# Performance work log

Measured on AMD Instinct MI355X. Metric: run time of the kernel, lower is better.

The kernel has to match this reference:

```python
import jax, jax.numpy as jnp
import numpy as np

N = 50000
E = 800000
NODE_DIM = 128
EDGE_DIM = 64


def leaky_relu(x, slope=0.2):
    return jnp.where(x >= 0, x, slope * x)


def setup_inputs() -> dict:
    key = jax.random.key(0)
    ks = jax.random.split(key, 12)
    node_feats = jax.random.normal(ks[0], (N, NODE_DIM), dtype=jnp.float32)
    edge_index = jax.random.randint(ks[1], (2, E), 0, N, dtype=jnp.int64)
    edge_feats = jax.random.normal(ks[2], (E, EDGE_DIM), dtype=jnp.float32)
    # msg_mlp: Linear(node+edge -> node), LeakyReLU(0.2), Linear(node -> node)
    s1 = 1.0 / np.sqrt(NODE_DIM + EDGE_DIM)
    s2 = 1.0 / np.sqrt(NODE_DIM)
    s3 = 1.0 / np.sqrt(2 * NODE_DIM)
    msg_w1 = jax.random.uniform(ks[3], (NODE_DIM + EDGE_DIM, NODE_DIM), jnp.float32, -s1, s1)
    msg_b1 = jax.random.uniform(ks[4], (NODE_DIM,), jnp.float32, -s1, s1)
    msg_w2 = jax.random.uniform(ks[5], (NODE_DIM, NODE_DIM), jnp.float32, -s2, s2)
    msg_b2 = jax.random.uniform(ks[6], (NODE_DIM,), jnp.float32, -s2, s2)
    # update_mlp: Linear(2*node -> node), LeakyReLU(0.2), Linear(node -> node)
    upd_w1 = jax.random.uniform(ks[7], (2 * NODE_DIM, NODE_DIM), jnp.float32, -s3, s3)
    upd_b1 = jax.random.uniform(ks[8], (NODE_DIM,), jnp.float32, -s3, s3)
    upd_w2 = jax.random.uniform(ks[9], (NODE_DIM, NODE_DIM), jnp.float32, -s2, s2)
    upd_b2 = jax.random.uniform(ks[10], (NODE_DIM,), jnp.float32, -s2, s2)
    return {
        "node_feats": node_feats,
        "edge_feats": edge_feats,
        "msg_w1": msg_w1, "msg_b1": msg_b1, "msg_w2": msg_w2, "msg_b2": msg_b2,
        "upd_w1": upd_w1, "upd_b1": upd_b1, "upd_w2": upd_w2, "upd_b2": upd_b2,
        "edge_index": edge_index,
    }


def reference(node_feats, edge_feats, msg_w1, msg_b1, msg_w2, msg_b2,
              upd_w1, upd_b1, upd_w2, upd_b2, edge_index):
    src = edge_index[0]
    dst = edge_index[1]
    # gather neighbor features, concat with edge features: (E, node+edge)
    msg_input = jnp.concatenate([node_feats[dst], edge_feats], axis=1)
    h = leaky_relu(msg_input @ msg_w1 + msg_b1)
    messages = h @ msg_w2 + msg_b2                       # (E, node_dim)
    # scatter-add messages to source nodes
    aggregated = jax.ops.segment_sum(messages, src, num_segments=node_feats.shape[0])
    update_input = jnp.concatenate([node_feats, aggregated], axis=1)  # (N, 2*node_dim)
    h2 = leaky_relu(update_input @ upd_w1 + upd_b1)
    return h2 @ upd_w2 + upd_b2                          # (N, node_dim)
```

## Files before the change

### kernel.cpp

```cpp
#include <hip/hip_runtime.h>
#include <hip/hip_bf16.h>

#define NNODES 50000
#define NEDGES 800000
#define NDIM   128
#define EDIM   64
#define K1     192
#define K2     256
#define NB     196

#define KP1 200
#define KPA 136
#define KPU 264
#define MSTR 132

typedef __attribute__((ext_vector_type(8))) short bf16x8;
typedef __attribute__((ext_vector_type(4))) short bf16x4;
typedef __attribute__((ext_vector_type(4))) float f32x4;

__device__ inline short f2bf(float f) {
  union { float f; unsigned u; } v; v.f = f;
  unsigned r = v.u + 0x7FFFu + ((v.u >> 16) & 1u);
  return (short)(r >> 16);
}

__device__ inline bf16x4 pack4(float4 v) {
  bf16x4 p;
  p[0] = f2bf(v.x); p[1] = f2bf(v.y); p[2] = f2bf(v.z); p[3] = f2bf(v.w);
  return p;
}

__global__ __launch_bounds__(256) void cvt_kernel(const float* __restrict__ src,
                                                  short* __restrict__ dst, int n) {
  int i = (blockIdx.x * 256 + threadIdx.x) * 4;
  if (i < n) {
    float4 v = *(const float4*)(src + i);
    *(bf16x4*)(dst + i) = pack4(v);
  }
}

__global__ __launch_bounds__(256) void wt_all_kernel(const float* __restrict__ w1,
                                                     const float* __restrict__ w2,
                                                     const float* __restrict__ u1,
                                                     const float* __restrict__ u2,
                                                     short* __restrict__ w1t,
                                                     short* __restrict__ w2t,
                                                     short* __restrict__ u1t,
                                                     short* __restrict__ u2t) {
  int i = blockIdx.x * 256 + threadIdx.x;
  const int A0 = K1 * 128;
  const int A1 = A0 + 128 * 128;
  const int A2 = A1 + K2 * 128;
  const int A3 = A2 + 128 * 128;
  if (i < A0) {
    int j = i, k = j >> 7, n = j & 127;
    w1t[n * K1 + k] = f2bf(w1[j]);
  } else if (i < A1) {
    int j = i - A0, k = j >> 7, n = j & 127;
    w2t[n * NDIM + k] = f2bf(w2[j]);
  } else if (i < A2) {
    int j = i - A1, k = j >> 7, n = j & 127;
    u1t[n * K2 + k] = f2bf(u1[j]);
  } else if (i < A3) {
    int j = i - A2, k = j >> 7, n = j & 127;
    u2t[n * NDIM + k] = f2bf(u2[j]);
  }
}

__global__ __launch_bounds__(256) void hist_kernel(const int* __restrict__ eidx,
                                                   int* __restrict__ cnt) {
  int i = blockIdx.x * 256 + threadIdx.x;
  if (i < NEDGES) atomicAdd(&cnt[eidx[i]], 1);
}

__global__ __launch_bounds__(256) void scan_reduce_kernel(const int* __restrict__ cnt,
                                                          int* __restrict__ bsum) {
  __shared__ int sh[256];
  int tid = threadIdx.x;
  int i = blockIdx.x * 256 + tid;
  sh[tid] = (i < NNODES) ? cnt[i] : 0;
  __syncthreads();
#pragma unroll
  for (int off = 128; off > 0; off >>= 1) {
    if (tid < off) sh[tid] += sh[tid + off];
    __syncthreads();
  }
  if (tid == 0) bsum[blockIdx.x] = sh[0];
}

__global__ __launch_bounds__(256) void scan_top_kernel(const int* __restrict__ bsum,
                                                       int* __restrict__ bscan) {
  __shared__ int sh[256];
  int tid = threadIdx.x;
  int v = (tid < NB) ? bsum[tid] : 0;
  sh[tid] = v;
  __syncthreads();
#pragma unroll
  for (int off = 1; off < 256; off <<= 1) {
    int t = (tid >= off) ? sh[tid - off] : 0;
    __syncthreads();
    sh[tid] += t;
    __syncthreads();
  }
  bscan[tid] = sh[tid] - v;
}

__global__ __launch_bounds__(256) void scan_down_kernel(int* __restrict__ cnt,
                                                        const int* __restrict__ bscan,
                                                        int* __restrict__ row_ptr) {
  __shared__ int sh[256];
  int tid = threadIdx.x;
  int i = blockIdx.x * 256 + tid;
  int v = (i < NNODES) ? cnt[i] : 0;
  sh[tid] = v;
  __syncthreads();
#pragma unroll
  for (int off = 1; off < 256; off <<= 1) {
    int t = (tid >= off) ? sh[tid - off] : 0;
    __syncthreads();
    sh[tid] += t;
    __syncthreads();
  }
  if (i < NNODES) {
    row_ptr[i] = bscan[blockIdx.x] + (sh[tid] - v);
    cnt[i] = 0;
  }
}

__global__ __launch_bounds__(256) void permute_kernel(const int* __restrict__ eidx,
                                                      const int* __restrict__ row_ptr,
                                                      int* __restrict__ cnt,
                                                      int4* __restrict__ s_edges) {
  int e = blockIdx.x * 256 + threadIdx.x;
  if (e < NEDGES) {
    int s = eidx[e];
    int d = eidx[NEDGES + e];
    int pos = row_ptr[s] + atomicAdd(&cnt[s], 1);
    s_edges[pos] = make_int4(s, d, e, 0);
  }
}

__global__ __launch_bounds__(256, 6) void edge_kernel(const short* __restrict__ nf_bf,
                                                      const float* __restrict__ edge_feats,
                                                      const int4* __restrict__ s_edges,
                                                      const short* __restrict__ w1t,
                                                      const float* __restrict__ b1,
                                                      float* __restrict__ hagg) {
  __shared__ __align__(16) char SH[64 * KP1 * 2];
  __shared__ int srcs[64];

  short* X = (short*)SH;
  float* M = (float*)SH;

  const int tid = threadIdx.x;
  const int e0 = blockIdx.x * 64;

  {
    int r = tid >> 2, q = tid & 3;
    int4 v = s_edges[e0 + r];
    if (q == 0) srcs[r] = v.x;
    const bf16x8* np = (const bf16x8*)(nf_bf + (size_t)v.y * NDIM) + q * 4;
    const float4* ep = (const float4*)(edge_feats + (size_t)v.z * EDIM) + q * 4;
    short* dpn = X + r * KP1 + q * 32;
    short* dpe = X + r * KP1 + NDIM + q * 16;
#pragma unroll
    for (int j = 0; j < 4; ++j) *(bf16x8*)(dpn + j * 8) = np[j];
#pragma unroll
    for (int j = 0; j < 4; ++j) *(bf16x4*)(dpe + j * 4) = pack4(ep[j]);
  }
  __syncthreads();

  const int lane = tid & 63;
  const int wv = tid >> 6;
  const int m16 = lane & 15;
  const int quad = lane >> 4;

  f32x4 acc[4][2];
#pragma unroll
  for (int mt = 0; mt < 4; ++mt)
#pragma unroll
    for (int nt = 0; nt < 2; ++nt)
      acc[mt][nt] = (f32x4){0.f, 0.f, 0.f, 0.f};

#pragma unroll
  for (int ks = 0; ks < 6; ++ks) {
    const int k0 = ks * 32 + quad * 8;
    bf16x8 b[2];
#pragma unroll
    for (int nt = 0; nt < 2; ++nt) {
      int n = wv * 32 + nt * 16 + m16;
      b[nt] = *(const bf16x8*)(w1t + n * K1 + k0);
    }
#pragma unroll
    for (int mt = 0; mt < 4; ++mt) {
      bf16x8 a = *(const bf16x8*)(X + (mt * 16 + m16) * KP1 + k0);
#pragma unroll
      for (int nt = 0; nt < 2; ++nt)
        acc[mt][nt] = __builtin_amdgcn_mfma_f32_16x16x32_bf16(a, b[nt], acc[mt][nt], 0, 0, 0);
    }
  }
  __syncthreads();

#pragma unroll
  for (int h = 0; h < 2; ++h) {
#pragma unroll
    for (int nt = 0; nt < 2; ++nt) {
      int col = wv * 32 + nt * 16 + m16;
      float bb = b1[col];
#pragma unroll
      for (int mt2 = 0; mt2 < 2; ++mt2) {
        int mt = h * 2 + mt2;
#pragma unroll
        for (int i = 0; i < 4; ++i) {
          float v = acc[mt][nt][i] + bb;
          v = v >= 0.f ? v : 0.2f * v;
          int lr = mt2 * 16 + quad * 4 + i;
          M[lr * MSTR + col] = v;
        }
      }
    }
    __syncthreads();
    {
      const int c = tid & 127;
      const int lr0 = (tid >> 7) * 16;
      const int g0 = h * 32 + lr0;
      float a = M[lr0 * MSTR + c];
      int prev = srcs[g0];
#pragma unroll 4
      for (int r = 1; r < 16; ++r) {
        int s = srcs[g0 + r];
        float v = M[(lr0 + r) * MSTR + c];
        if (s != prev) {
          atomicAdd(&hagg[(size_t)prev * NDIM + c], a);
          a = v;
          prev = s;
        } else {
          a += v;
        }
      }
      atomicAdd(&hagg[(size_t)prev * NDIM + c], a);
    }
    if (h == 0) __syncthreads();
  }
}

__global__ __launch_bounds__(256) void node_kernel(const short* __restrict__ nf_bf,
                                                   const float* __restrict__ hagg,
                                                   const int* __restrict__ degc,
                                                   const short* __restrict__ w2t,
                                                   const float* __restrict__ b2,
                                                   const short* __restrict__ u1t,
                                                   const float* __restrict__ ub1,
                                                   const short* __restrict__ u2t,
                                                   const float* __restrict__ ub2,
                                                   float* __restrict__ out) {
  __shared__ __align__(16) short AGH[32 * KPA];
  __shared__ __align__(16) short XU[32 * KPU];
  __shared__ float degs[32];

  const int tid = threadIdx.x;
  const int n0 = blockIdx.x * 32;

  if (tid < 32) {
    int node = n0 + tid;
    degs[tid] = (node < NNODES) ? (float)degc[node] : 0.f;
  }
  {
    int r = tid >> 3, q = tid & 7;
    int node = n0 + r; if (node >= NNODES) node = NNODES - 1;
    const float4* hp = (const float4*)(hagg + (size_t)node * NDIM) + q * 4;
    const bf16x8* xp = (const bf16x8*)(nf_bf + (size_t)node * NDIM) + q * 2;
    short* ap = AGH + r * KPA + q * 16;
    short* xq = XU + r * KPU + q * 16;
#pragma unroll
    for (int j = 0; j < 4; ++j) *(bf16x4*)(ap + j * 4) = pack4(hp[j]);
#pragma unroll
    for (int j = 0; j < 2; ++j) *(bf16x8*)(xq + j * 8) = xp[j];
  }
  __syncthreads();

  const int lane = tid & 63;
  const int wv = tid >> 6;
  const int m16 = lane & 15;
  const int quad = lane >> 4;

  f32x4 acc[2][2];

#pragma unroll
  for (int mt = 0; mt < 2; ++mt)
#pragma unroll
    for (int nt = 0; nt < 2; ++nt)
      acc[mt][nt] = (f32x4){0.f, 0.f, 0.f, 0.f};
#pragma unroll
  for (int ks = 0; ks < 4; ++ks) {
    const int k0 = ks * 32 + quad * 8;
    bf16x8 b[2];
#pragma unroll
    for (int nt = 0; nt < 2; ++nt) {
      int n = wv * 32 + nt * 16 + m16;
      b[nt] = *(const bf16x8*)(w2t + n * NDIM + k0);
    }
#pragma unroll
    for (int mt = 0; mt < 2; ++mt) {
      bf16x8 a = *(const bf16x8*)(AGH + (mt * 16 + m16) * KPA + k0);
#pragma unroll
      for (int nt = 0; nt < 2; ++nt)
        acc[mt][nt] = __builtin_amdgcn_mfma_f32_16x16x32_bf16(a, b[nt], acc[mt][nt], 0, 0, 0);
    }
  }
#pragma unroll
  for (int nt = 0; nt < 2; ++nt) {
    int col = wv * 32 + nt * 16 + m16;
    float bb = b2[col];
#pragma unroll
    for (int mt = 0; mt < 2; ++mt) {
#pragma unroll
      for (int i = 0; i < 4; ++i) {
        int row = mt * 16 + quad * 4 + i;
        float v = acc[mt][nt][i] + degs[row] * bb;
        XU[row * KPU + NDIM + col] = f2bf(v);
      }
    }
  }
  __syncthreads();

#pragma unroll
  for (int mt = 0; mt < 2; ++mt)
#pragma unroll
    for (int nt = 0; nt < 2; ++nt)
      acc[mt][nt] = (f32x4){0.f, 0.f, 0.f, 0.f};
#pragma unroll
  for (int ks = 0; ks < 8; ++ks) {
    const int k0 = ks * 32 + quad * 8;
    bf16x8 b[2];
#pragma unroll
    for (int nt = 0; nt < 2; ++nt) {
      int n = wv * 32 + nt * 16 + m16;
      b[nt] = *(const bf16x8*)(u1t + n * K2 + k0);
    }
#pragma unroll
    for (int mt = 0; mt < 2; ++mt) {
      bf16x8 a = *(const bf16x8*)(XU + (mt * 16 + m16) * KPU + k0);
#pragma unroll
      for (int nt = 0; nt < 2; ++nt)
        acc[mt][nt] = __builtin_amdgcn_mfma_f32_16x16x32_bf16(a, b[nt], acc[mt][nt], 0, 0, 0);
    }
  }
  __syncthreads();
#pragma unroll
  for (int nt = 0; nt < 2; ++nt) {
    int col = wv * 32 + nt * 16 + m16;
    float bb = ub1[col];
#pragma unroll
    for (int mt = 0; mt < 2; ++mt) {
#pragma unroll
      for (int i = 0; i < 4; ++i) {
        int row = mt * 16 + quad * 4 + i;
        float v = acc[mt][nt][i] + bb;
        v = v >= 0.f ? v : 0.2f * v;
        AGH[row * KPA + col] = f2bf(v);
      }
    }
  }
  __syncthreads();

#pragma unroll
  for (int mt = 0; mt < 2; ++mt)
#pragma unroll
    for (int nt = 0; nt < 2; ++nt)
      acc[mt][nt] = (f32x4){0.f, 0.f, 0.f, 0.f};
#pragma unroll
  for (int ks = 0; ks < 4; ++ks) {
    const int k0 = ks * 32 + quad * 8;
    bf16x8 b[2];
#pragma unroll
    for (int nt = 0; nt < 2; ++nt) {
      int n = wv * 32 + nt * 16 + m16;
      b[nt] = *(const bf16x8*)(u2t + n * NDIM + k0);
    }
#pragma unroll
    for (int mt = 0; mt < 2; ++mt) {
      bf16x8 a = *(const bf16x8*)(AGH + (mt * 16 + m16) * KPA + k0);
#pragma unroll
      for (int nt = 0; nt < 2; ++nt)
        acc[mt][nt] = __builtin_amdgcn_mfma_f32_16x16x32_bf16(a, b[nt], acc[mt][nt], 0, 0, 0);
    }
  }
#pragma unroll
  for (int nt = 0; nt < 2; ++nt) {
    int col = wv * 32 + nt * 16 + m16;
    float bb = ub2[col];
#pragma unroll
    for (int mt = 0; mt < 2; ++mt) {
#pragma unroll
      for (int i = 0; i < 4; ++i) {
        int row = mt * 16 + quad * 4 + i;
        int node = n0 + row;
        if (node < NNODES)
          out[(size_t)node * NDIM + col] = acc[mt][nt][i] + bb;
      }
    }
  }
}

extern "C" void kernel_launch(void* const* d_in, const int* in_sizes, int n_in,
                              void* d_out, int out_size, void* d_ws, size_t ws_size,
                              hipStream_t stream) {
  const float* node_feats = (const float*)d_in[0];
  const float* edge_feats = (const float*)d_in[1];
  const float* msg_w1 = (const float*)d_in[2];
  const float* msg_b1 = (const float*)d_in[3];
  const float* msg_w2 = (const float*)d_in[4];
  const float* msg_b2 = (const float*)d_in[5];
  const float* upd_w1 = (const float*)d_in[6];
  const float* upd_b1 = (const float*)d_in[7];
  const float* upd_w2 = (const float*)d_in[8];
  const float* upd_b2 = (const float*)d_in[9];
  const int* eidx = (const int*)d_in[10];

  float* hagg   = (float*)d_ws;
  int* cnt      = (int*)(hagg + (size_t)NNODES * NDIM);
  int* row_ptr  = cnt + NNODES;
  int* bsum     = row_ptr + NNODES;
  int* bscan    = bsum + 256;
  int4* s_edges = (int4*)(bscan + 256);
  short* w1t    = (short*)(s_edges + NEDGES);
  short* w2t    = w1t + 128 * K1;
  short* u1t    = w2t + 128 * 128;
  short* u2t    = u1t + 128 * K2;
  short* nf_bf  = u2t + 128 * 128;

  hipMemsetAsync(d_ws, 0, (size_t)(NNODES * NDIM + NNODES) * sizeof(float), stream);

  cvt_kernel<<<(NNODES * NDIM / 4 + 255) / 256, 256, 0, stream>>>(node_feats, nf_bf,
                                                                  NNODES * NDIM);
  wt_all_kernel<<<(90112 + 255) / 256, 256, 0, stream>>>(msg_w1, msg_w2, upd_w1, upd_w2,
                                                         w1t, w2t, u1t, u2t);

  hist_kernel<<<NEDGES / 256, 256, 0, stream>>>(eidx, cnt);
  scan_reduce_kernel<<<NB, 256, 0, stream>>>(cnt, bsum);
  scan_top_kernel<<<1, 256, 0, stream>>>(bsum, bscan);
  scan_down_kernel<<<NB, 256, 0, stream>>>(cnt, bscan, row_ptr);
  permute_kernel<<<NEDGES / 256, 256, 0, stream>>>(eidx, row_ptr, cnt, s_edges);

  edge_kernel<<<NEDGES / 64, 256, 0, stream>>>(nf_bf, edge_feats, s_edges,
                                               w1t, msg_b1, hagg);
  node_kernel<<<(NNODES + 31) / 32, 256, 0, stream>>>(nf_bf, hagg, cnt,
                                                      w2t, msg_b2, u1t, upd_b1,
                                                      u2t, upd_b2, (float*)d_out);
}
```

Measured before the change: 530.2 us.

## Load edge rows directly into MFMA registers and stage swizzled weights in LDS

The edge kernel no longer gathers node and edge features into shared memory. Each lane loads its A-operand fragments straight from global memory into registers. The full W1 matrix is instead staged in LDS with an XOR swizzle, and each wave computes all 128 output columns for its own 16 rows. The segmented scatter-add now runs from accumulator registers, combining only 4 rows per lane before the atomics. This drops the LDS round trip and the extra barriers, but issues more atomics per edge group and lowers the occupancy hint from 6 to 3 blocks per CU.

```diff
diff --git a/kernel.cpp b/kernel.cpp
--- a/kernel.cpp
+++ b/kernel.cpp
@@ -9,10 +9,8 @@
 #define K2     256
 #define NB     196
 
-#define KP1 200
 #define KPA 136
 #define KPU 264
-#define MSTR 132
 
 typedef __attribute__((ext_vector_type(8))) short bf16x8;
 typedef __attribute__((ext_vector_type(4))) short bf16x4;
@@ -140,107 +138,91 @@
   }
 }
 
-__global__ __launch_bounds__(256, 6) void edge_kernel(const short* __restrict__ nf_bf,
+__global__ __launch_bounds__(256, 3) void edge_kernel(const short* __restrict__ nf_bf,
                                                       const float* __restrict__ edge_feats,
                                                       const int4* __restrict__ s_edges,
                                                       const short* __restrict__ w1t,
                                                       const float* __restrict__ b1,
                                                       float* __restrict__ hagg) {
-  __shared__ __align__(16) char SH[64 * KP1 * 2];
-  __shared__ int srcs[64];
-
-  short* X = (short*)SH;
-  float* M = (float*)SH;
+  __shared__ __align__(16) short B[128 * K1];
 
   const int tid = threadIdx.x;
   const int e0 = blockIdx.x * 64;
-
-  {
-    int r = tid >> 2, q = tid & 3;
-    int4 v = s_edges[e0 + r];
-    if (q == 0) srcs[r] = v.x;
-    const bf16x8* np = (const bf16x8*)(nf_bf + (size_t)v.y * NDIM) + q * 4;
-    const float4* ep = (const float4*)(edge_feats + (size_t)v.z * EDIM) + q * 4;
-    short* dpn = X + r * KP1 + q * 32;
-    short* dpe = X + r * KP1 + NDIM + q * 16;
-#pragma unroll
-    for (int j = 0; j < 4; ++j) *(bf16x8*)(dpn + j * 8) = np[j];
-#pragma unroll
-    for (int j = 0; j < 4; ++j) *(bf16x4*)(dpe + j * 4) = pack4(ep[j]);
-  }
-  __syncthreads();
-
   const int lane = tid & 63;
   const int wv = tid >> 6;
   const int m16 = lane & 15;
   const int quad = lane >> 4;
 
-  f32x4 acc[4][2];
-#pragma unroll
-  for (int mt = 0; mt < 4; ++mt)
-#pragma unroll
-    for (int nt = 0; nt < 2; ++nt)
-      acc[mt][nt] = (f32x4){0.f, 0.f, 0.f, 0.f};
-
+  const int row = (wv << 4) + m16;
+  const int4 rec = s_edges[e0 + row];
+  bf16x8 a[6];
+  {
+    const short* np = nf_bf + (size_t)rec.y * NDIM + quad * 8;
+#pragma unroll
+    for (int ks = 0; ks < 4; ++ks) a[ks] = *(const bf16x8*)(np + ks * 32);
+    const float* ep = edge_feats + (size_t)rec.z * EDIM + quad * 8;
+#pragma unroll
+    for (int ks = 0; ks < 2; ++ks) {
+      float4 lo = *(const float4*)(ep + ks * 32);
+      float4 hi = *(const float4*)(ep + ks * 32 + 4);
+      bf16x4 pl = pack4(lo), ph = pack4(hi);
+      bf16x8 p;
+      p[0] = pl[0]; p[1] = pl[1]; p[2] = pl[2]; p[3] = pl[3];
+      p[4] = ph[0]; p[5] = ph[1]; p[6] = ph[2]; p[7] = ph[3];
+      a[4 + ks] = p;
+    }
+  }
+  const int* sp = (const int*)(s_edges + e0 + (wv << 4) + (quad << 2));
+  const int sa = sp[0], sb = sp[4], sc = sp[8], sd = sp[12];
+  float bias[8];
+#pragma unroll
+  for (int nt = 0; nt < 8; ++nt) bias[nt] = b1[nt * 16 + m16];
+
+  {
+    const int n = tid >> 1;
+    const int h = tid & 1;
+    const short* src = w1t + n * K1 + h * 96;
+    short* drow = B + n * K1;
+    const int x7 = n & 7;
+#pragma unroll
+    for (int j = 0; j < 12; ++j) {
+      const int s = h * 12 + j;
+      *(bf16x8*)(drow + ((s ^ x7) << 3)) = *(const bf16x8*)(src + j * 8);
+    }
+  }
+  __syncthreads();
+
+  f32x4 acc[8];
+#pragma unroll
+  for (int nt = 0; nt < 8; ++nt) acc[nt] = (f32x4){0.f, 0.f, 0.f, 0.f};
+  const int x7 = m16 & 7;
 #pragma unroll
   for (int ks = 0; ks < 6; ++ks) {
-    const int k0 = ks * 32 + quad * 8;
-    bf16x8 b[2];
-#pragma unroll
-    for (int nt = 0; nt < 2; ++nt) {
-      int n = wv * 32 + nt * 16 + m16;
-      b[nt] = *(const bf16x8*)(w1t + n * K1 + k0);
-    }
-#pragma unroll
-    for (int mt = 0; mt < 4; ++mt) {
-      bf16x8 a = *(const bf16x8*)(X + (mt * 16 + m16) * KP1 + k0);
-#pragma unroll
-      for (int nt = 0; nt < 2; ++nt)
-        acc[mt][nt] = __builtin_amdgcn_mfma_f32_16x16x32_bf16(a, b[nt], acc[mt][nt], 0, 0, 0);
-    }
-  }
-  __syncthreads();
-
-#pragma unroll
-  for (int h = 0; h < 2; ++h) {
-#pragma unroll
-    for (int nt = 0; nt < 2; ++nt) {
-      int col = wv * 32 + nt * 16 + m16;
-      float bb = b1[col];
-#pragma unroll
-      for (int mt2 = 0; mt2 < 2; ++mt2) {
-        int mt = h * 2 + mt2;
-#pragma unroll
-        for (int i = 0; i < 4; ++i) {
-          float v = acc[mt][nt][i] + bb;
-          v = v >= 0.f ? v : 0.2f * v;
-          int lr = mt2 * 16 + quad * 4 + i;
-          M[lr * MSTR + col] = v;
-        }
-      }
-    }
-    __syncthreads();
-    {
-      const int c = tid & 127;
-      const int lr0 = (tid >> 7) * 16;
-      const int g0 = h * 32 + lr0;
-      float a = M[lr0 * MSTR + c];
-      int prev = srcs[g0];
-#pragma unroll 4
-      for (int r = 1; r < 16; ++r) {
-        int s = srcs[g0 + r];
-        float v = M[(lr0 + r) * MSTR + c];
-        if (s != prev) {
-          atomicAdd(&hagg[(size_t)prev * NDIM + c], a);
-          a = v;
-          prev = s;
-        } else {
-          a += v;
-        }
-      }
-      atomicAdd(&hagg[(size_t)prev * NDIM + c], a);
-    }
-    if (h == 0) __syncthreads();
+    const int so = ((ks * 4 + quad) ^ x7) << 3;
+#pragma unroll
+    for (int nt = 0; nt < 8; ++nt) {
+      bf16x8 b = *(const bf16x8*)(B + (nt * 16 + m16) * K1 + so);
+      acc[nt] = __builtin_amdgcn_mfma_f32_16x16x32_bf16(a[ks], b, acc[nt], 0, 0, 0);
+    }
+  }
+
+  const bool k1 = (sb != sa), k2 = (sc != sb), k3 = (sd != sc);
+#pragma unroll
+  for (int nt = 0; nt < 8; ++nt) {
+    const float bb = bias[nt];
+    float v0 = acc[nt][0] + bb; v0 = v0 >= 0.f ? v0 : 0.2f * v0;
+    float v1 = acc[nt][1] + bb; v1 = v1 >= 0.f ? v1 : 0.2f * v1;
+    float v2 = acc[nt][2] + bb; v2 = v2 >= 0.f ? v2 : 0.2f * v2;
+    float v3 = acc[nt][3] + bb; v3 = v3 >= 0.f ? v3 : 0.2f * v3;
+    const int c = nt * 16 + m16;
+    float run = v0; int prev = sa;
+    if (k1) { atomicAdd(&hagg[(size_t)prev * NDIM + c], run); run = v1; prev = sb; }
+    else    { run += v1; }
+    if (k2) { atomicAdd(&hagg[(size_t)prev * NDIM + c], run); run = v2; prev = sc; }
+    else    { run += v2; }
+    if (k3) { atomicAdd(&hagg[(size_t)prev * NDIM + c], run); run = v3; prev = sd; }
+    else    { run += v3; }
+    atomicAdd(&hagg[(size_t)prev * NDIM + c], run);
   }
 }
 
```

Measured after the change: 668.0 us. 26.0% more time.

## Make edge kernel persistent over four tiles with register prefetch and swizzled LDS

Applied to the files above, without the earlier changes.

Each edge block now handles four 64-edge tiles instead of one. W1 fragments and bias are loaded into registers once per block and reused across the tiles. The next tile's gathered node and edge features are prefetched into registers while the current tile's MFMAs run, with double-buffered node LDS and an XOR swizzle in place of row padding to avoid bank conflicts. The cost is higher register pressure (launch bound lowered to 3 waves per EU) and four times fewer blocks, which reduces parallel slack.

```diff
diff --git a/kernel.cpp b/kernel.cpp
--- a/kernel.cpp
+++ b/kernel.cpp
@@ -8,11 +8,10 @@
 #define K1     192
 #define K2     256
 #define NB     196
-
-#define KP1 200
+#define TPB_E  4
+
 #define KPA 136
 #define KPU 264
-#define MSTR 132
 
 typedef __attribute__((ext_vector_type(8))) short bf16x8;
 typedef __attribute__((ext_vector_type(4))) short bf16x4;
@@ -28,6 +27,12 @@
   bf16x4 p;
   p[0] = f2bf(v.x); p[1] = f2bf(v.y); p[2] = f2bf(v.z); p[3] = f2bf(v.w);
   return p;
+}
+
+__device__ inline void wg_barrier_lds() {
+  asm volatile("s_waitcnt lgkmcnt(0)" ::: "memory");
+  __builtin_amdgcn_s_barrier();
+  asm volatile("" ::: "memory");
 }
 
 __global__ __launch_bounds__(256) void cvt_kernel(const float* __restrict__ src,
@@ -140,107 +145,149 @@
   }
 }
 
-__global__ __launch_bounds__(256, 6) void edge_kernel(const short* __restrict__ nf_bf,
+__global__ __launch_bounds__(256, 3) void edge_kernel(const short* __restrict__ nf_bf,
                                                       const float* __restrict__ edge_feats,
                                                       const int4* __restrict__ s_edges,
                                                       const short* __restrict__ w1t,
                                                       const float* __restrict__ b1,
                                                       float* __restrict__ hagg) {
-  __shared__ __align__(16) char SH[64 * KP1 * 2];
+  __shared__ __align__(16) short XN[2][64 * 128];
+  __shared__ __align__(16) short XE[64 * 64];
   __shared__ int srcs[64];
 
-  short* X = (short*)SH;
-  float* M = (float*)SH;
-
   const int tid = threadIdx.x;
-  const int e0 = blockIdx.x * 64;
-
-  {
-    int r = tid >> 2, q = tid & 3;
-    int4 v = s_edges[e0 + r];
-    if (q == 0) srcs[r] = v.x;
-    const bf16x8* np = (const bf16x8*)(nf_bf + (size_t)v.y * NDIM) + q * 4;
-    const float4* ep = (const float4*)(edge_feats + (size_t)v.z * EDIM) + q * 4;
-    short* dpn = X + r * KP1 + q * 32;
-    short* dpe = X + r * KP1 + NDIM + q * 16;
-#pragma unroll
-    for (int j = 0; j < 4; ++j) *(bf16x8*)(dpn + j * 8) = np[j];
-#pragma unroll
-    for (int j = 0; j < 4; ++j) *(bf16x4*)(dpe + j * 4) = pack4(ep[j]);
-  }
-  __syncthreads();
-
   const int lane = tid & 63;
   const int wv = tid >> 6;
   const int m16 = lane & 15;
   const int quad = lane >> 4;
-
-  f32x4 acc[4][2];
-#pragma unroll
-  for (int mt = 0; mt < 4; ++mt)
+  const int r = tid >> 2, q = tid & 3;
+  const int rx = r & 7;
+  const int mx = m16 & 7;
+
+  const int e0 = blockIdx.x * (64 * TPB_E);
+
+  float bias[2];
+#pragma unroll
+  for (int nt = 0; nt < 2; ++nt) bias[nt] = b1[wv * 32 + nt * 16 + m16];
+
+  bf16x8 bfrag[6][2];
+#pragma unroll
+  for (int ks = 0; ks < 6; ++ks)
 #pragma unroll
     for (int nt = 0; nt < 2; ++nt)
-      acc[mt][nt] = (f32x4){0.f, 0.f, 0.f, 0.f};
-
-#pragma unroll
-  for (int ks = 0; ks < 6; ++ks) {
-    const int k0 = ks * 32 + quad * 8;
-    bf16x8 b[2];
-#pragma unroll
-    for (int nt = 0; nt < 2; ++nt) {
-      int n = wv * 32 + nt * 16 + m16;
-      b[nt] = *(const bf16x8*)(w1t + n * K1 + k0);
-    }
-#pragma unroll
-    for (int mt = 0; mt < 4; ++mt) {
-      bf16x8 a = *(const bf16x8*)(X + (mt * 16 + m16) * KP1 + k0);
-#pragma unroll
-      for (int nt = 0; nt < 2; ++nt)
-        acc[mt][nt] = __builtin_amdgcn_mfma_f32_16x16x32_bf16(a, b[nt], acc[mt][nt], 0, 0, 0);
-    }
-  }
-  __syncthreads();
-
-#pragma unroll
-  for (int h = 0; h < 2; ++h) {
-#pragma unroll
-    for (int nt = 0; nt < 2; ++nt) {
-      int col = wv * 32 + nt * 16 + m16;
-      float bb = b1[col];
-#pragma unroll
-      for (int mt2 = 0; mt2 < 2; ++mt2) {
-        int mt = h * 2 + mt2;
-#pragma unroll
-        for (int i = 0; i < 4; ++i) {
-          float v = acc[mt][nt][i] + bb;
-          v = v >= 0.f ? v : 0.2f * v;
-          int lr = mt2 * 16 + quad * 4 + i;
-          M[lr * MSTR + col] = v;
+      bfrag[ks][nt] = *(const bf16x8*)(w1t + (wv * 32 + nt * 16 + m16) * K1 + ks * 32 + quad * 8);
+
+  int4 rec = s_edges[e0 + r];
+  bf16x8 pn[4];
+  float4 pe[4];
+  {
+    const bf16x8* np = (const bf16x8*)(nf_bf + (size_t)rec.y * NDIM) + q * 4;
+#pragma unroll
+    for (int j = 0; j < 4; ++j) pn[j] = np[j];
+    const float4* ep = (const float4*)(edge_feats + (size_t)rec.z * EDIM) + q * 4;
+#pragma unroll
+    for (int j = 0; j < 4; ++j) pe[j] = ep[j];
+  }
+
+  for (int t = 0; t < TPB_E; ++t) {
+    short* xn = XN[t & 1];
+
+    {
+      short* rowp = xn + r * 128;
+#pragma unroll
+      for (int j = 0; j < 4; ++j)
+        *(bf16x8*)(rowp + (((q * 4 + j) ^ rx) << 3)) = pn[j];
+      bf16x4 c0 = pack4(pe[0]), c1 = pack4(pe[1]), c2 = pack4(pe[2]), c3 = pack4(pe[3]);
+      bf16x8 p0, p1;
+      p0[0]=c0[0]; p0[1]=c0[1]; p0[2]=c0[2]; p0[3]=c0[3];
+      p0[4]=c1[0]; p0[5]=c1[1]; p0[6]=c1[2]; p0[7]=c1[3];
+      p1[0]=c2[0]; p1[1]=c2[1]; p1[2]=c2[2]; p1[3]=c2[3];
+      p1[4]=c3[0]; p1[5]=c3[1]; p1[6]=c3[2]; p1[7]=c3[3];
+      short* erow = XE + r * 64;
+      *(bf16x8*)(erow + (((q * 2 + 0) ^ rx) << 3)) = p0;
+      *(bf16x8*)(erow + (((q * 2 + 1) ^ rx) << 3)) = p1;
+      if (q == 0) srcs[r] = rec.x;
+    }
+    __syncthreads();
+
+    if (t + 1 < TPB_E) {
+      rec = s_edges[e0 + (t + 1) * 64 + r];
+      const bf16x8* np = (const bf16x8*)(nf_bf + (size_t)rec.y * NDIM) + q * 4;
+#pragma unroll
+      for (int j = 0; j < 4; ++j) pn[j] = np[j];
+      const float4* ep = (const float4*)(edge_feats + (size_t)rec.z * EDIM) + q * 4;
+#pragma unroll
+      for (int j = 0; j < 4; ++j) pe[j] = ep[j];
+    }
+
+    f32x4 acc[4][2];
+#pragma unroll
+    for (int mt = 0; mt < 4; ++mt)
+#pragma unroll
+      for (int nt = 0; nt < 2; ++nt) acc[mt][nt] = (f32x4){0.f, 0.f, 0.f, 0.f};
+#pragma unroll
+    for (int ks = 0; ks < 4; ++ks) {
+#pragma unroll
+      for (int mt = 0; mt < 4; ++mt) {
+        bf16x8 a = *(const bf16x8*)(xn + (mt * 16 + m16) * 128 + (((ks * 4 + quad) ^ mx) << 3));
+#pragma unroll
+        for (int nt = 0; nt < 2; ++nt)
+          acc[mt][nt] = __builtin_amdgcn_mfma_f32_16x16x32_bf16(a, bfrag[ks][nt], acc[mt][nt], 0, 0, 0);
+      }
+    }
+#pragma unroll
+    for (int ks = 4; ks < 6; ++ks) {
+#pragma unroll
+      for (int mt = 0; mt < 4; ++mt) {
+        bf16x8 a = *(const bf16x8*)(XE + (mt * 16 + m16) * 64 + ((((ks - 4) * 4 + quad) ^ mx) << 3));
+#pragma unroll
+        for (int nt = 0; nt < 2; ++nt)
+          acc[mt][nt] = __builtin_amdgcn_mfma_f32_16x16x32_bf16(a, bfrag[ks][nt], acc[mt][nt], 0, 0, 0);
+      }
+    }
+    wg_barrier_lds();
+
+    float* M = (float*)xn;
+#pragma unroll
+    for (int h = 0; h < 2; ++h) {
+#pragma unroll
+      for (int nt = 0; nt < 2; ++nt) {
+        const int col = wv * 32 + nt * 16 + m16;
+        const float bb = bias[nt];
+#pragma unroll
+        for (int mt2 = 0; mt2 < 2; ++mt2) {
+          const int mt = h * 2 + mt2;
+#pragma unroll
+          for (int i = 0; i < 4; ++i) {
+            float v = acc[mt][nt][i] + bb;
+            v = v >= 0.f ? v : 0.2f * v;
+            M[(mt2 * 16 + quad * 4 + i) * 128 + col] = v;
+          }
         }
       }
-    }
-    __syncthreads();
-    {
-      const int c = tid & 127;
-      const int lr0 = (tid >> 7) * 16;
-      const int g0 = h * 32 + lr0;
-      float a = M[lr0 * MSTR + c];
-      int prev = srcs[g0];
+      wg_barrier_lds();
+      {
+        const int c = tid & 127;
+        const int lr0 = (tid >> 7) * 16;
+        const int g0 = h * 32 + lr0;
+        float a = M[lr0 * 128 + c];
+        int prev = srcs[g0];
 #pragma unroll 4
-      for (int r = 1; r < 16; ++r) {
-        int s = srcs[g0 + r];
-        float v = M[(lr0 + r) * MSTR + c];
-        if (s != prev) {
-          atomicAdd(&hagg[(size_t)prev * NDIM + c], a);
-          a = v;
-          prev = s;
-        } else {
-          a += v;
+        for (int rr = 1; rr < 16; ++rr) {
+          int s = srcs[g0 + rr];
+          float v = M[(lr0 + rr) * 128 + c];
+          if (s != prev) {
+            atomicAdd(&hagg[(size_t)prev * NDIM + c], a);
+            a = v;
+            prev = s;
+          } else {
+            a += v;
+          }
         }
-      }
-      atomicAdd(&hagg[(size_t)prev * NDIM + c], a);
-    }
-    if (h == 0) __syncthreads();
+        atomicAdd(&hagg[(size_t)prev * NDIM + c], a);
+      }
+      wg_barrier_lds();
+    }
   }
 }
 
@@ -443,8 +490,8 @@
   scan_down_kernel<<<NB, 256, 0, stream>>>(cnt, bscan, row_ptr);
   permute_kernel<<<NEDGES / 256, 256, 0, stream>>>(eidx, row_ptr, cnt, s_edges);
 
-  edge_kernel<<<NEDGES / 64, 256, 0, stream>>>(nf_bf, edge_feats, s_edges,
-                                               w1t, msg_b1, hagg);
+  edge_kernel<<<NEDGES / (64 * TPB_E), 256, 0, stream>>>(nf_bf, edge_feats, s_edges,
+                                                         w1t, msg_b1, hagg);
   node_kernel<<<(NNODES + 31) / 32, 256, 0, stream>>>(nf_bf, hagg, cnt,
                                                       w2t, msg_b2, u1t, upd_b1,
                                                       u2t, upd_b2, (float*)d_out);
```

Result: faster. 507.3 us (-4.3%).
